# Optimization experiments

Hardware: AMD Instinct MI355X
Metric: run time of the kernel (lower is better)

Reference implementation:

```python
import jax, jax.numpy as jnp
import numpy as np
from jax import lax

WORDS_NUM = 1024   # N
WORD_SIZE = 128    # W
READ_HEADS = 4     # R
BATCH = 32
SEQ = 512
D_IN = 512
IFACE = WORD_SIZE * READ_HEADS + 3 * WORD_SIZE + 5 * READ_HEADS + 3  # 919


def _l2norm(v, axis):
    s = jnp.sum(v * v, axis=axis, keepdims=True)
    return v * lax.rsqrt(jnp.maximum(s, 1e-12))


def _lookup(memory, keys, strengths):
    # memory: (B,N,W), keys: (B,W,K), strengths: (B,K) -> (B,N,K)
    nm = _l2norm(memory, 2)
    nk = _l2norm(keys, 1)
    sim = jnp.einsum('bnw,bwk->bnk', nm, nk)
    return jax.nn.softmax(sim * strengths[:, None, :], axis=1)


def setup_inputs() -> dict:
    key = jax.random.key(0)
    kx, kw = jax.random.split(key)
    x = jax.random.normal(kx, (BATCH, SEQ, D_IN), jnp.float32)
    limit = float(np.sqrt(6.0 / (D_IN + IFACE)))  # glorot_uniform
    interface_weights = jax.random.uniform(kw, (D_IN, IFACE), jnp.float32, -limit, limit)
    return {'x': x, 'interface_weights': interface_weights}


def reference(x, interface_weights):
    B, N, W, R = BATCH, WORDS_NUM, WORD_SIZE, READ_HEADS
    # initial DNC state (as in __init__)
    memory0 = jnp.full((B, N, W), 1e-6, jnp.float32)
    usage0 = jnp.zeros((B, N), jnp.float32)
    prec0 = jnp.zeros((B, N), jnp.float32)
    link0 = jnp.zeros((B, N, N), jnp.float32)
    ww0 = jnp.full((B, N), 1e-6, jnp.float32)
    rw0 = jnp.full((B, N, R), 1e-6, jnp.float32)
    eye = jnp.eye(N, dtype=jnp.float32)

    # interface: dense + global average pool over sequence
    iface = jnp.mean(x @ interface_weights, axis=1)  # (B, IFACE)

    # ---- parse interface vector ----
    r_keys_end = W * R
    r_str_end = r_keys_end + R
    w_key_end = r_str_end + W
    erase_end = w_key_end + 1 + W
    write_end = erase_end + W
    free_end = write_end + R
    read_keys = iface[:, :r_keys_end].reshape(B, W, R)
    read_strengths = 1.0 + jax.nn.softplus(iface[:, r_keys_end:r_str_end])   # (B,R)
    write_key = iface[:, r_str_end:w_key_end].reshape(B, W, 1)
    write_strength = 1.0 + jax.nn.softplus(iface[:, w_key_end][:, None])     # (B,1)
    erase_vector = jax.nn.sigmoid(iface[:, w_key_end + 1:erase_end])         # (B,W)
    write_vector = iface[:, erase_end:write_end]                             # (B,W)
    free_gates = jax.nn.sigmoid(iface[:, write_end:free_end])               # (B,R)
    allocation_gate = jax.nn.sigmoid(iface[:, free_end][:, None])            # (B,1)
    write_gate = jax.nn.sigmoid(iface[:, free_end + 1][:, None])             # (B,1)
    read_modes = jax.nn.softmax(iface[:, free_end + 2:].reshape(B, 3, R), axis=1)

    # ---- read (uses previous memory / link, as in call(): read before write) ----
    lookup_r = _lookup(memory0, read_keys, read_strengths)       # (B,N,R)
    fwd_w = jnp.einsum('bnm,bmr->bnr', link0, rw0)
    bwd_w = jnp.einsum('bmn,bmr->bnr', link0, rw0)
    rw = (read_modes[:, 0][:, None, :] * bwd_w
          + read_modes[:, 1][:, None, :] * lookup_r
          + read_modes[:, 2][:, None, :] * fwd_w)                 # (B,N,R)
    read_vectors = jnp.einsum('bnw,bnr->bwr', memory0, rw)        # (B,W,R)
    out = read_vectors.reshape(B, W * R)

    # ---- write ----
    lookup_w = _lookup(memory0, write_key, write_strength)[:, :, 0]  # (B,N)
    retention = jnp.prod(1.0 - free_gates[:, None, :] * rw, axis=2)  # (B,N)
    usage = (usage0 + ww0 - usage0 * ww0) * retention
    neg_sorted, free_list = lax.top_k(-usage, N)
    sorted_usage = -neg_sorted
    cp = jnp.cumprod(sorted_usage, axis=1)                           # exclusive cumprod
    shifted = jnp.concatenate([jnp.ones((B, 1), jnp.float32), cp[:, :-1]], axis=1)
    unordered = (1.0 - sorted_usage) * shifted
    alloc = jnp.zeros((B, N), jnp.float32).at[jnp.arange(B)[:, None], free_list].set(unordered)
    ww = write_gate * (allocation_gate * alloc + (1.0 - allocation_gate) * lookup_w)
    memory = memory0 * (1.0 - ww[:, :, None] * erase_vector[:, None, :]) \
             + ww[:, :, None] * write_vector[:, None, :]
    link = ((1.0 - ww[:, :, None] - ww[:, None, :]) * link0
            + ww[:, :, None] * prec0[:, None, :]) * (1.0 - eye)
    prec = (1.0 - jnp.sum(ww, axis=1, keepdims=True)) * prec0 + ww

    return (out, memory, link, usage, prec, ww, rw)
```

## Files before the change

kernel.cpp:

```cpp
#include <hip/hip_runtime.h>
#include <math.h>

#define BATCH 32
#define SEQ   512
#define DIN   512
#define IFACE 919
#define NW    1024
#define WS    128
#define RH    4

#define TAILC 274
#define TAIL0 645

#define XM_PART 0
#define IFC     262144
#define EVO     270912
#define WVO     275008
#define WWH     279104
#define SCAL    281152
#define RWV     281408

#define OUT_OFF   0
#define MEM_OFF   16384
#define LINK_OFF  4210688
#define USAGE_OFF 37765120
#define PREC_OFF  37797888
#define WW_OFF    37830656
#define RW_OFF    37863424

__device__ __forceinline__ float sigmoidf_(float x) { return 1.0f / (1.0f + expf(-x)); }

__global__ void k_zero_link(float4* __restrict__ dst, int count4) {
    int idx = blockIdx.x * blockDim.x + threadIdx.x;
    int stride = gridDim.x * blockDim.x;
    float4 z = {0.f, 0.f, 0.f, 0.f};
    for (int i = idx; i < count4; i += stride) dst[i] = z;
}

__global__ void k_reduce_x(const float* __restrict__ x, float* __restrict__ ws) {
    int c = blockIdx.x, b = blockIdx.y, t = threadIdx.x;
    const float4* xr = (const float4*)(x + (size_t)(b * SEQ + c * 32) * DIN);
    float4 acc = {0.f, 0.f, 0.f, 0.f};
    for (int s = 0; s < 32; ++s) {
        float4 v = xr[s * 128 + t];
        acc.x += v.x; acc.y += v.y; acc.z += v.z; acc.w += v.w;
    }
    ((float4*)(ws + XM_PART))[(b * 16 + c) * 128 + t] = acc;
}

__global__ void k_iface(float* __restrict__ ws, const float* __restrict__ Wif) {
    __shared__ float xms[DIN];
    int b = blockIdx.y, t = threadIdx.x;
    for (int d = t; d < DIN; d += 256) {
        const float* p = ws + XM_PART + (size_t)b * 16 * DIN + d;
        float s = 0.f;
        #pragma unroll
        for (int c = 0; c < 16; ++c) s += p[c * DIN];
        xms[d] = s;
    }
    __syncthreads();
    int j = blockIdx.x * 256 + t;
    if (j >= TAILC) return;
    float acc = 0.f;
    for (int k = 0; k < DIN; ++k) acc += xms[k] * Wif[k * IFACE + TAIL0 + j];
    ws[IFC + b * TAILC + j] = acc * (1.0f / SEQ);
}

__global__ void k_params(float* __restrict__ ws, float* __restrict__ out) {
    int b = blockIdx.x, t = threadIdx.x;
    const float* p = ws + IFC + b * TAILC;

    ws[EVO + b * 128 + t] = sigmoidf_(p[t]);
    ws[WVO + b * 128 + t] = p[128 + t];

    float rm1[RH];
    #pragma unroll
    for (int r = 0; r < RH; ++r) {
        float i0 = p[262 + r], i1 = p[266 + r], i2 = p[270 + r];
        float mx = fmaxf(i0, fmaxf(i1, i2));
        float e0 = expf(i0 - mx), e1 = expf(i1 - mx), e2 = expf(i2 - mx);
        rm1[r] = e1 / (e0 + e1 + e2);
    }

    float4 o = {1e-6f * rm1[0], 1e-6f * rm1[1], 1e-6f * rm1[2], 1e-6f * rm1[3]};
    ((float4*)(out + OUT_OFF))[b * 128 + t] = o;

    if (t == 0) {
        const float inv1024 = 1.0f / 1024.0f;
        float ret = 1.f;
        #pragma unroll
        for (int r = 0; r < RH; ++r) {
            float rwv = rm1[r] * inv1024;
            ws[RWV + b * 4 + r] = rwv;
            float fg = sigmoidf_(p[256 + r]);
            ret *= (1.f - fg * rwv);
        }
        float u = 1e-6f * ret;
        float ag = sigmoidf_(p[260]);
        float wg = sigmoidf_(p[261]);
        float wwc = wg * (ag * 0.0f + (1.f - ag) * inv1024);
        ws[SCAL + b * 8 + 0] = u;
        ws[SCAL + b * 8 + 1] = wwc;
        float cum = 1.f;
        for (int n = 0; n < 64; ++n) {
            float alloc = (1.f - u) * cum;
            ws[WWH + b * 64 + n] = wg * (ag * alloc + (1.f - ag) * inv1024);
            cum *= u;
        }
    }
}

__global__ void k_memory(const float* __restrict__ ws, float* __restrict__ out) {
    int idx = blockIdx.x * 256 + threadIdx.x;
    int w4 = idx & 31;
    int n  = (idx >> 5) & 1023;
    int b  = idx >> 15;
    float ww = (n < 64) ? ws[WWH + b * 64 + n] : ws[SCAL + b * 8 + 1];
    float4 e = ((const float4*)(ws + EVO))[b * 32 + w4];
    float4 v = ((const float4*)(ws + WVO))[b * 32 + w4];
    float4 m;
    m.x = 1e-6f * (1.f - ww * e.x) + ww * v.x;
    m.y = 1e-6f * (1.f - ww * e.y) + ww * v.y;
    m.z = 1e-6f * (1.f - ww * e.z) + ww * v.z;
    m.w = 1e-6f * (1.f - ww * e.w) + ww * v.w;
    ((float4*)(out + MEM_OFF))[idx] = m;
}

__global__ void k_small(const float* __restrict__ ws, float* __restrict__ out) {
    int t = blockIdx.x * 256 + threadIdx.x;
    int b = t >> 10, n = t & 1023;
    float u  = ws[SCAL + b * 8 + 0];
    float ww = (n < 64) ? ws[WWH + b * 64 + n] : ws[SCAL + b * 8 + 1];
    out[USAGE_OFF + t] = u;
    out[PREC_OFF + t]  = ww;
    out[WW_OFF + t]    = ww;
    float4 rv = ((const float4*)(ws + RWV))[b];
    ((float4*)out)[RW_OFF / 4 + t] = rv;
}

extern "C" void kernel_launch(void* const* d_in, const int* in_sizes, int n_in,
                              void* d_out, int out_size, void* d_ws, size_t ws_size,
                              hipStream_t stream) {
    const float* x   = (const float*)d_in[0];
    const float* Wif = (const float*)d_in[1];
    float* out = (float*)d_out;
    float* ws  = (float*)d_ws;

    k_zero_link<<<8192, 256, 0, stream>>>((float4*)(out + LINK_OFF), 33554432 / 4);
    k_reduce_x<<<dim3(16, 32), 128, 0, stream>>>(x, ws);
    k_iface<<<dim3(2, 32), 256, 0, stream>>>(ws, Wif);
    k_params<<<32, 128, 0, stream>>>(ws, out);
    k_memory<<<4096, 256, 0, stream>>>(ws, out);
    k_small<<<128, 256, 0, stream>>>(ws, out);
}
```

Before: 69.01 us.

## Fuse six kernels into three, overlapping link zeroing with x reduction

Merges the link-zeroing kernel and the x sequence reduction into one launch, so the 134MB zero fill and the x read share a grid and overlap. The interface projection, parameter computation and small-output writes move into one per-batch kernel, removing three launches and workspace round trips. The trade-off is that the iface matvec now runs in only 32 blocks instead of 64, which serialises more work per block.

```diff
diff --git a/kernel.cpp b/kernel.cpp
--- a/kernel.cpp
+++ b/kernel.cpp
@@ -5,20 +5,14 @@
 #define SEQ   512
 #define DIN   512
 #define IFACE 919
-#define NW    1024
-#define WS    128
-#define RH    4
-
 #define TAILC 274
 #define TAIL0 645
 
 #define XM_PART 0
-#define IFC     262144
-#define EVO     270912
-#define WVO     275008
-#define WWH     279104
-#define SCAL    281152
-#define RWV     281408
+#define EVO     262144
+#define WVO     266240
+#define WWH     270336
+#define SCAL    272384
 
 #define OUT_OFF   0
 #define MEM_OFF   16384
@@ -28,94 +22,126 @@
 #define WW_OFF    37830656
 #define RW_OFF    37863424
 
+#define LINK4     8388608
+#define ZBLOCKS   4096
+#define RBLOCKS   512
+
 __device__ __forceinline__ float sigmoidf_(float x) { return 1.0f / (1.0f + expf(-x)); }
 
-__global__ void k_zero_link(float4* __restrict__ dst, int count4) {
-    int idx = blockIdx.x * blockDim.x + threadIdx.x;
-    int stride = gridDim.x * blockDim.x;
-    float4 z = {0.f, 0.f, 0.f, 0.f};
-    for (int i = idx; i < count4; i += stride) dst[i] = z;
+__global__ void kA(const float* __restrict__ x, float* __restrict__ ws,
+                   float4* __restrict__ link) {
+    int bid = blockIdx.x;
+    if (bid < RBLOCKS) {
+        int b = bid >> 4, c = bid & 15, t = threadIdx.x;
+        int half = t >> 7, d4 = t & 127;
+        __shared__ float4 tmp[128];
+        const float4* xr = (const float4*)(x + (size_t)((b * SEQ) + c * 32 + half * 16) * DIN);
+        float4 acc = {0.f, 0.f, 0.f, 0.f};
+        #pragma unroll
+        for (int s = 0; s < 16; ++s) {
+            float4 v = xr[s * 128 + d4];
+            acc.x += v.x; acc.y += v.y; acc.z += v.z; acc.w += v.w;
+        }
+        if (half == 1) tmp[d4] = acc;
+        __syncthreads();
+        if (half == 0) {
+            float4 o = tmp[d4];
+            acc.x += o.x; acc.y += o.y; acc.z += o.z; acc.w += o.w;
+            ((float4*)(ws + XM_PART))[(b * 16 + c) * 128 + d4] = acc;
+        }
+    } else {
+        int idx = (bid - RBLOCKS) * 256 + threadIdx.x;
+        int stride = ZBLOCKS * 256;
+        float4 z = {0.f, 0.f, 0.f, 0.f};
+        for (int i = idx; i < LINK4; i += stride) link[i] = z;
+    }
 }
 
-__global__ void k_reduce_x(const float* __restrict__ x, float* __restrict__ ws) {
-    int c = blockIdx.x, b = blockIdx.y, t = threadIdx.x;
-    const float4* xr = (const float4*)(x + (size_t)(b * SEQ + c * 32) * DIN);
-    float4 acc = {0.f, 0.f, 0.f, 0.f};
-    for (int s = 0; s < 32; ++s) {
-        float4 v = xr[s * 128 + t];
-        acc.x += v.x; acc.y += v.y; acc.z += v.z; acc.w += v.w;
-    }
-    ((float4*)(ws + XM_PART))[(b * 16 + c) * 128 + t] = acc;
-}
+__global__ void kB(float* __restrict__ ws, const float* __restrict__ Wif,
+                   float* __restrict__ out) {
+    __shared__ float xms[DIN];
+    __shared__ float p[TAILC];
+    __shared__ float s_u, s_wwc, s_wwh[64];
+    int b = blockIdx.x, t = threadIdx.x;
 
-__global__ void k_iface(float* __restrict__ ws, const float* __restrict__ Wif) {
-    __shared__ float xms[DIN];
-    int b = blockIdx.y, t = threadIdx.x;
     for (int d = t; d < DIN; d += 256) {
-        const float* p = ws + XM_PART + (size_t)b * 16 * DIN + d;
+        const float* q = ws + XM_PART + (size_t)b * 16 * DIN + d;
         float s = 0.f;
         #pragma unroll
-        for (int c = 0; c < 16; ++c) s += p[c * DIN];
+        for (int c = 0; c < 16; ++c) s += q[c * DIN];
         xms[d] = s;
     }
     __syncthreads();
-    int j = blockIdx.x * 256 + t;
-    if (j >= TAILC) return;
-    float acc = 0.f;
-    for (int k = 0; k < DIN; ++k) acc += xms[k] * Wif[k * IFACE + TAIL0 + j];
-    ws[IFC + b * TAILC + j] = acc * (1.0f / SEQ);
-}
 
-__global__ void k_params(float* __restrict__ ws, float* __restrict__ out) {
-    int b = blockIdx.x, t = threadIdx.x;
-    const float* p = ws + IFC + b * TAILC;
+    for (int j = t; j < TAILC; j += 256) {
+        const float* wcol = Wif + TAIL0 + j;
+        float acc = 0.f;
+        #pragma unroll 8
+        for (int k = 0; k < DIN; ++k) acc += xms[k] * wcol[(size_t)k * IFACE];
+        p[j] = acc * (1.0f / SEQ);
+    }
+    __syncthreads();
 
-    ws[EVO + b * 128 + t] = sigmoidf_(p[t]);
-    ws[WVO + b * 128 + t] = p[128 + t];
-
-    float rm1[RH];
+    float rm1[4];
     #pragma unroll
-    for (int r = 0; r < RH; ++r) {
+    for (int r = 0; r < 4; ++r) {
         float i0 = p[262 + r], i1 = p[266 + r], i2 = p[270 + r];
         float mx = fmaxf(i0, fmaxf(i1, i2));
         float e0 = expf(i0 - mx), e1 = expf(i1 - mx), e2 = expf(i2 - mx);
         rm1[r] = e1 / (e0 + e1 + e2);
     }
 
-    float4 o = {1e-6f * rm1[0], 1e-6f * rm1[1], 1e-6f * rm1[2], 1e-6f * rm1[3]};
-    ((float4*)(out + OUT_OFF))[b * 128 + t] = o;
+    if (t < 128) {
+        ws[EVO + b * 128 + t] = sigmoidf_(p[t]);
+        ws[WVO + b * 128 + t] = p[128 + t];
+        float4 o = {1e-6f * rm1[0], 1e-6f * rm1[1], 1e-6f * rm1[2], 1e-6f * rm1[3]};
+        ((float4*)(out + OUT_OFF))[b * 128 + t] = o;
+    }
 
     if (t == 0) {
         const float inv1024 = 1.0f / 1024.0f;
         float ret = 1.f;
         #pragma unroll
-        for (int r = 0; r < RH; ++r) {
-            float rwv = rm1[r] * inv1024;
-            ws[RWV + b * 4 + r] = rwv;
+        for (int r = 0; r < 4; ++r) {
             float fg = sigmoidf_(p[256 + r]);
-            ret *= (1.f - fg * rwv);
+            ret *= (1.f - fg * rm1[r] * inv1024);
         }
         float u = 1e-6f * ret;
         float ag = sigmoidf_(p[260]);
         float wg = sigmoidf_(p[261]);
-        float wwc = wg * (ag * 0.0f + (1.f - ag) * inv1024);
-        ws[SCAL + b * 8 + 0] = u;
-        ws[SCAL + b * 8 + 1] = wwc;
+        float wwc = wg * (1.f - ag) * inv1024;
+        s_u = u; s_wwc = wwc;
+        ws[SCAL + b * 2 + 0] = u;
+        ws[SCAL + b * 2 + 1] = wwc;
         float cum = 1.f;
         for (int n = 0; n < 64; ++n) {
             float alloc = (1.f - u) * cum;
-            ws[WWH + b * 64 + n] = wg * (ag * alloc + (1.f - ag) * inv1024);
+            float w = wg * (ag * alloc + (1.f - ag) * inv1024);
+            s_wwh[n] = w;
+            ws[WWH + b * 64 + n] = w;
             cum *= u;
         }
     }
+    __syncthreads();
+
+    float u = s_u;
+    float4 rv = {rm1[0] * (1.0f / 1024.0f), rm1[1] * (1.0f / 1024.0f),
+                 rm1[2] * (1.0f / 1024.0f), rm1[3] * (1.0f / 1024.0f)};
+    for (int n = t; n < 1024; n += 256) {
+        float ww = (n < 64) ? s_wwh[n] : s_wwc;
+        out[USAGE_OFF + b * 1024 + n] = u;
+        out[PREC_OFF + b * 1024 + n] = ww;
+        out[WW_OFF + b * 1024 + n] = ww;
+        ((float4*)out)[RW_OFF / 4 + b * 1024 + n] = rv;
+    }
 }
 
-__global__ void k_memory(const float* __restrict__ ws, float* __restrict__ out) {
+__global__ void kC(const float* __restrict__ ws, float* __restrict__ out) {
     int idx = blockIdx.x * 256 + threadIdx.x;
     int w4 = idx & 31;
     int n  = (idx >> 5) & 1023;
     int b  = idx >> 15;
-    float ww = (n < 64) ? ws[WWH + b * 64 + n] : ws[SCAL + b * 8 + 1];
+    float ww = (n < 64) ? ws[WWH + b * 64 + n] : ws[SCAL + b * 2 + 1];
     float4 e = ((const float4*)(ws + EVO))[b * 32 + w4];
     float4 v = ((const float4*)(ws + WVO))[b * 32 + w4];
     float4 m;
@@ -126,18 +152,6 @@
     ((float4*)(out + MEM_OFF))[idx] = m;
 }
 
-__global__ void k_small(const float* __restrict__ ws, float* __restrict__ out) {
-    int t = blockIdx.x * 256 + threadIdx.x;
-    int b = t >> 10, n = t & 1023;
-    float u  = ws[SCAL + b * 8 + 0];
-    float ww = (n < 64) ? ws[WWH + b * 64 + n] : ws[SCAL + b * 8 + 1];
-    out[USAGE_OFF + t] = u;
-    out[PREC_OFF + t]  = ww;
-    out[WW_OFF + t]    = ww;
-    float4 rv = ((const float4*)(ws + RWV))[b];
-    ((float4*)out)[RW_OFF / 4 + t] = rv;
-}
-
 extern "C" void kernel_launch(void* const* d_in, const int* in_sizes, int n_in,
                               void* d_out, int out_size, void* d_ws, size_t ws_size,
                               hipStream_t stream) {
@@ -146,10 +160,7 @@
     float* out = (float*)d_out;
     float* ws  = (float*)d_ws;
 
-    k_zero_link<<<8192, 256, 0, stream>>>((float4*)(out + LINK_OFF), 33554432 / 4);
-    k_reduce_x<<<dim3(16, 32), 128, 0, stream>>>(x, ws);
-    k_iface<<<dim3(2, 32), 256, 0, stream>>>(ws, Wif);
-    k_params<<<32, 128, 0, stream>>>(ws, out);
-    k_memory<<<4096, 256, 0, stream>>>(ws, out);
-    k_small<<<128, 256, 0, stream>>>(ws, out);
+    kA<<<RBLOCKS + ZBLOCKS, 256, 0, stream>>>(x, ws, (float4*)(out + LINK_OFF));
+    kB<<<32, 256, 0, stream>>>(ws, Wif, out);
+    kC<<<4096, 256, 0, stream>>>(ws, out);
 }
```

Result: slower. 85.53 us (+23.9%).
